# Kernel optimization log

Hardware: AMD Instinct MI355X
Metric: run time of the kernel (lower is better)

Reference implementation:

```python
import jax, jax.numpy as jnp
import numpy as np

KEY_DIM, VALUE_DIM, N_ACTIONS = 128, 64, 256
B, L = 32, 2048


def setup_inputs() -> dict:
    key = jax.random.key(0)
    k1, k2, k3 = jax.random.split(key, 3)
    key_vectors = jax.random.normal(k1, (B, L, KEY_DIM), dtype=jnp.float32)
    value_vectors = jax.random.normal(k2, (B, N_ACTIONS, KEY_DIM), dtype=jnp.float32)
    weights = jax.random.normal(k3, (KEY_DIM, VALUE_DIM, N_ACTIONS), dtype=jnp.float32)
    return {"key_vectors": key_vectors, "value_vectors": value_vectors, "weights": weights}


def reference(key_vectors, value_vectors, weights):
    # torch: einsum('bln,nka->bla', key, W) sums over both n (key_dim) and k (value_dim)
    scores = jnp.einsum('bln,nka->bla', key_vectors, weights)  # (B, L, A)
    # fused multiply-then-reduce over actions == batched matmul (no (B,L,A,D) intermediate)
    mem_vectors = jnp.einsum('bla,bad->bld', scores, value_vectors)  # (B, L, key_dim)
    q_values = jnp.einsum('bln,bmn->blm', key_vectors, mem_vectors)  # (B, L, L)
    return q_values
```

## Files before the change

### kernel.cpp

```cpp
#include <hip/hip_runtime.h>
#include <hip/hip_bf16.h>

#define KD 128
#define VD 64
#define NA 256
#define NB 32
#define LL 2048

typedef __attribute__((ext_vector_type(8))) short bf16x8;
typedef __attribute__((ext_vector_type(4))) float f32x4;
typedef __attribute__((ext_vector_type(8))) unsigned short u16x8;
typedef __attribute__((ext_vector_type(4))) unsigned short u16x4;

static __device__ __forceinline__ unsigned short f2bf(float x) {
  __hip_bfloat16 h = __float2bfloat16(x);
  unsigned short u;
  __builtin_memcpy(&u, &h, 2);
  return u;
}

static __device__ __forceinline__ void stage16(const void* gsrc, void* ldst) {
  __builtin_amdgcn_global_load_lds(
      (const __attribute__((address_space(1))) void*)gsrc,
      (__attribute__((address_space(3))) void*)ldst, 16, 0, 0);
}

__global__ __launch_bounds__(256) void fold_w(const float* __restrict__ W,
                                              float* __restrict__ W2) {
  const int idx = blockIdx.x * 256 + threadIdx.x;
  const int n = idx >> 8, a = idx & 255;
  const float* p = W + (long)n * (VD * NA) + a;
  float s = 0.f;
  #pragma unroll
  for (int k = 0; k < VD; ++k) s += p[k * NA];
  W2[idx] = s;
}

__global__ __launch_bounds__(128) void compute_t(const float* __restrict__ W2,
                                                 const float* __restrict__ V,
                                                 unsigned short* __restrict__ Tt) {
  const int n = threadIdx.x;
  const int d0 = blockIdx.x * 8;
  const int b = blockIdx.y;
  const float* vb = V + (long)b * NA * KD + d0;
  const float* w2p = W2 + n * NA;
  float acc[8] = {0.f, 0.f, 0.f, 0.f, 0.f, 0.f, 0.f, 0.f};
  for (int a = 0; a < NA; a += 4) {
    const float4 w = *(const float4*)(w2p + a);
    const float wq[4] = {w.x, w.y, w.z, w.w};
    #pragma unroll
    for (int q = 0; q < 4; ++q) {
      const float* vr = vb + (long)(a + q) * KD;
      #pragma unroll
      for (int j = 0; j < 8; ++j) acc[j] += wq[q] * vr[j];
    }
  }
  #pragma unroll
  for (int j = 0; j < 8; ++j)
    Tt[((long)b * KD + d0 + j) * KD + n] = f2bf(acc[j]);
}

__global__ __launch_bounds__(256) void cvt_key(const float* __restrict__ in,
                                               unsigned short* __restrict__ out) {
  const long i = ((long)blockIdx.x * 256 + threadIdx.x) * 8;
  const float4 f0 = *(const float4*)(in + i);
  const float4 f1 = *(const float4*)(in + i + 4);
  u16x8 r;
  r[0] = f2bf(f0.x); r[1] = f2bf(f0.y); r[2] = f2bf(f0.z); r[3] = f2bf(f0.w);
  r[4] = f2bf(f1.x); r[5] = f2bf(f1.y); r[6] = f2bf(f1.z); r[7] = f2bf(f1.w);
  *(u16x8*)(out + i) = r;
}

__global__ __launch_bounds__(256) void gemm_mem(const unsigned short* __restrict__ A,
                                                const unsigned short* __restrict__ Bm,
                                                unsigned short* __restrict__ C) {
  __shared__ unsigned short lds[32768];
  const int nper = gridDim.x >> 3;
  const int lg = (blockIdx.x & 7) * nper + (blockIdx.x >> 3);
  const int mt = lg & 15;
  const int b = lg >> 4;

  const int tid = threadIdx.x;
  const int lane = tid & 63, w = tid >> 6;
  const int l15 = lane & 15, lhi = lane >> 4;

  const unsigned short* gA = A + ((long)b * LL + mt * 128) * KD;
  const unsigned short* gB = Bm + (long)b * KD * KD;

  unsigned short* ldsA = lds;
  unsigned short* ldsB = lds + 16384;

  #pragma unroll
  for (int i = 0; i < 8; ++i) {
    const int addr = (w * 8 + i) * 1024 + lane * 16;
    const int row = addr >> 8;
    const int src = addr ^ ((row & 7) << 4);
    stage16((const char*)gA + src, (char*)ldsA + addr);
    stage16((const char*)gB + src, (char*)ldsB + addr);
  }
  __syncthreads();

  const int wr = w >> 1, wc = w & 1;
  f32x4 acc[4][4];
  #pragma unroll
  for (int i = 0; i < 4; ++i)
    #pragma unroll
    for (int j = 0; j < 4; ++j) acc[i][j] = f32x4{0.f, 0.f, 0.f, 0.f};

  #pragma unroll
  for (int ks = 0; ks < 4; ++ks) {
    const int kb = (ks * 32 + lhi * 8) * 2;
    bf16x8 av[4], bv[4];
    #pragma unroll
    for (int mf = 0; mf < 4; ++mf) {
      const int row = wr * 64 + mf * 16 + l15;
      const int byte = (row * 256 + kb) ^ ((row & 7) << 4);
      av[mf] = *(const bf16x8*)((const char*)ldsA + byte);
    }
    #pragma unroll
    for (int nf = 0; nf < 4; ++nf) {
      const int row = wc * 64 + nf * 16 + l15;
      const int byte = (row * 256 + kb) ^ ((row & 7) << 4);
      bv[nf] = *(const bf16x8*)((const char*)ldsB + byte);
    }
    #pragma unroll
    for (int mf = 0; mf < 4; ++mf)
      #pragma unroll
      for (int nf = 0; nf < 4; ++nf)
        acc[mf][nf] = __builtin_amdgcn_mfma_f32_16x16x32_bf16(bv[nf], av[mf],
                                                              acc[mf][nf], 0, 0, 0);
  }

  const long row0 = (long)b * LL + mt * 128 + wr * 64;
  const int col0 = wc * 64;
  #pragma unroll
  for (int mf = 0; mf < 4; ++mf)
    #pragma unroll
    for (int nf = 0; nf < 4; ++nf) {
      const long r = row0 + mf * 16 + l15;
      const int c = col0 + nf * 16 + lhi * 4;
      u16x4 v;
      #pragma unroll
      for (int i = 0; i < 4; ++i) v[i] = f2bf(acc[mf][nf][i]);
      *(u16x4*)(C + r * KD + c) = v;
    }
}

__global__ __launch_bounds__(512, 2) void gemm_q(const unsigned short* __restrict__ A,
                                                 const unsigned short* __restrict__ Bm,
                                                 float* __restrict__ C) {
  __shared__ unsigned short lds[65536];

  const int lg = (blockIdx.x & 7) * 256 + (blockIdx.x >> 3);
  const int nt = lg & 7;
  const int mt = (lg >> 3) & 7;
  const int b = lg >> 6;

  const int tid = threadIdx.x;
  const int lane = tid & 63, w = tid >> 6;
  const int l15 = lane & 15, lhi = lane >> 4;
  const int wrM = w >> 2;
  const int wcN = w & 3;

  const unsigned short* gA = A + ((long)b * LL + mt * 256) * KD;
  const unsigned short* gB = Bm + ((long)b * LL + nt * 256) * KD;

  unsigned short* ldsA = lds;
  unsigned short* ldsB = lds + 32768;

  #pragma unroll
  for (int i = 0; i < 8; ++i) {
    const int addr = i * 8192 + tid * 16;
    const int row = addr >> 8;
    const int src = addr ^ ((row & 7) << 4);
    stage16((const char*)gA + src, (char*)ldsA + addr);
    stage16((const char*)gB + src, (char*)ldsB + addr);
  }
  __syncthreads();

  f32x4 acc[8][4];
  #pragma unroll
  for (int i = 0; i < 8; ++i)
    #pragma unroll
    for (int j = 0; j < 4; ++j) acc[i][j] = f32x4{0.f, 0.f, 0.f, 0.f};

  #pragma unroll
  for (int ks = 0; ks < 4; ++ks) {
    const int kb = (ks * 32 + lhi * 8) * 2;
    bf16x8 av[8], bv[4];
    #pragma unroll
    for (int mf = 0; mf < 8; ++mf) {
      const int row = wrM * 128 + mf * 16 + l15;
      const int byte = (row * 256 + kb) ^ ((row & 7) << 4);
      av[mf] = *(const bf16x8*)((const char*)ldsA + byte);
    }
    #pragma unroll
    for (int nf = 0; nf < 4; ++nf) {
      const int row = wcN * 64 + nf * 16 + l15;
      const int byte = (row * 256 + kb) ^ ((row & 7) << 4);
      bv[nf] = *(const bf16x8*)((const char*)ldsB + byte);
    }
    #pragma unroll
    for (int mf = 0; mf < 8; ++mf)
      #pragma unroll
      for (int nf = 0; nf < 4; ++nf)
        acc[mf][nf] = __builtin_amdgcn_mfma_f32_16x16x32_bf16(bv[nf], av[mf],
                                                              acc[mf][nf], 0, 0, 0);
  }

  const long row0 = (long)b * LL + mt * 256 + wrM * 128;
  const int col0 = nt * 256 + wcN * 64;
  #pragma unroll
  for (int mf = 0; mf < 8; ++mf)
    #pragma unroll
    for (int nf = 0; nf < 4; ++nf) {
      const long r = row0 + mf * 16 + l15;
      const int c = col0 + nf * 16 + lhi * 4;
      *(f32x4*)(C + r * LL + c) = acc[mf][nf];
    }
}

extern "C" void kernel_launch(void* const* d_in, const int* in_sizes, int n_in,
                              void* d_out, int out_size, void* d_ws, size_t ws_size,
                              hipStream_t stream) {
  const float* key = (const float*)d_in[0];
  const float* val = (const float*)d_in[1];
  const float* wts = (const float*)d_in[2];
  float* out = (float*)d_out;

  char* ws = (char*)d_ws;
  float* W2 = (float*)ws;
  unsigned short* Tt = (unsigned short*)(ws + 131072);
  unsigned short* keyB = (unsigned short*)(ws + 131072 + 1048576);
  unsigned short* memB = (unsigned short*)(ws + 131072 + 1048576 + 16777216);

  fold_w<<<128, 256, 0, stream>>>(wts, W2);
  compute_t<<<dim3(16, NB), 128, 0, stream>>>(W2, val, Tt);
  cvt_key<<<4096, 256, 0, stream>>>(key, keyB);
  gemm_mem<<<16 * NB, 256, 0, stream>>>(keyB, Tt, memB);
  gemm_q<<<8 * 8 * NB, 512, 0, stream>>>(keyB, memB, out);
}
```

Baseline: 177.3 us.

## Make gemm_q persistent over M tiles, overlapping next A-tile load with stores

Each gemm_q block now keeps its B tile resident and loops over all eight M tiles of the batch, instead of launching one block per (M,N) tile. The next A tile is prefetched into LDS with global_load_lds while the current fp32 output tile is being written, so load latency is meant to hide behind the store-bound epilogue. This cuts the grid from 2048 to 256 blocks, which may underfill the CUs. The vmcnt-based wait also relies on an exact count of in-flight stores and loads.

```diff
diff --git a/kernel.cpp b/kernel.cpp
--- a/kernel.cpp
+++ b/kernel.cpp
@@ -149,12 +149,12 @@
 __global__ __launch_bounds__(512, 2) void gemm_q(const unsigned short* __restrict__ A,
                                                  const unsigned short* __restrict__ Bm,
                                                  float* __restrict__ C) {
-  __shared__ unsigned short lds[65536];
-
-  const int lg = (blockIdx.x & 7) * 256 + (blockIdx.x >> 3);
+  __shared__ unsigned short ldsA[32768];
+  __shared__ unsigned short ldsB[32768];
+
+  const int lg = (blockIdx.x & 7) * 32 + (blockIdx.x >> 3);
   const int nt = lg & 7;
-  const int mt = (lg >> 3) & 7;
-  const int b = lg >> 6;
+  const int b = lg >> 3;
 
   const int tid = threadIdx.x;
   const int lane = tid & 63, w = tid >> 6;
@@ -162,62 +162,87 @@
   const int wrM = w >> 2;
   const int wcN = w & 3;
 
-  const unsigned short* gA = A + ((long)b * LL + mt * 256) * KD;
   const unsigned short* gB = Bm + ((long)b * LL + nt * 256) * KD;
-
-  unsigned short* ldsA = lds;
-  unsigned short* ldsB = lds + 32768;
+  const unsigned short* gAb = A + (long)b * LL * KD;
 
   #pragma unroll
   for (int i = 0; i < 8; ++i) {
     const int addr = i * 8192 + tid * 16;
     const int row = addr >> 8;
     const int src = addr ^ ((row & 7) << 4);
-    stage16((const char*)gA + src, (char*)ldsA + addr);
     stage16((const char*)gB + src, (char*)ldsB + addr);
-  }
-  __syncthreads();
-
-  f32x4 acc[8][4];
-  #pragma unroll
-  for (int i = 0; i < 8; ++i)
-    #pragma unroll
-    for (int j = 0; j < 4; ++j) acc[i][j] = f32x4{0.f, 0.f, 0.f, 0.f};
-
-  #pragma unroll
-  for (int ks = 0; ks < 4; ++ks) {
-    const int kb = (ks * 32 + lhi * 8) * 2;
-    bf16x8 av[8], bv[4];
-    #pragma unroll
-    for (int mf = 0; mf < 8; ++mf) {
-      const int row = wrM * 128 + mf * 16 + l15;
-      const int byte = (row * 256 + kb) ^ ((row & 7) << 4);
-      av[mf] = *(const bf16x8*)((const char*)ldsA + byte);
-    }
-    #pragma unroll
-    for (int nf = 0; nf < 4; ++nf) {
-      const int row = wcN * 64 + nf * 16 + l15;
-      const int byte = (row * 256 + kb) ^ ((row & 7) << 4);
-      bv[nf] = *(const bf16x8*)((const char*)ldsB + byte);
-    }
+    stage16((const char*)gAb + src, (char*)ldsA + addr);
+  }
+  asm volatile("s_waitcnt vmcnt(0)" ::: "memory");
+  __builtin_amdgcn_s_barrier();
+  __builtin_amdgcn_sched_barrier(0);
+
+  const int col0 = nt * 256 + wcN * 64;
+
+  for (int mt = 0; mt < 8; ++mt) {
+    f32x4 acc[8][4];
+    #pragma unroll
+    for (int i = 0; i < 8; ++i)
+      #pragma unroll
+      for (int j = 0; j < 4; ++j) acc[i][j] = f32x4{0.f, 0.f, 0.f, 0.f};
+
+    #pragma unroll
+    for (int ks = 0; ks < 4; ++ks) {
+      const int kb = (ks * 32 + lhi * 8) * 2;
+      bf16x8 av[8], bv[4];
+      #pragma unroll
+      for (int mf = 0; mf < 8; ++mf) {
+        const int row = wrM * 128 + mf * 16 + l15;
+        const int byte = (row * 256 + kb) ^ ((row & 7) << 4);
+        av[mf] = *(const bf16x8*)((const char*)ldsA + byte);
+      }
+      #pragma unroll
+      for (int nf = 0; nf < 4; ++nf) {
+        const int row = wcN * 64 + nf * 16 + l15;
+        const int byte = (row * 256 + kb) ^ ((row & 7) << 4);
+        bv[nf] = *(const bf16x8*)((const char*)ldsB + byte);
+      }
+      #pragma unroll
+      for (int mf = 0; mf < 8; ++mf)
+        #pragma unroll
+        for (int nf = 0; nf < 4; ++nf)
+          acc[mf][nf] = __builtin_amdgcn_mfma_f32_16x16x32_bf16(bv[nf], av[mf],
+                                                                acc[mf][nf], 0, 0, 0);
+    }
+
+    asm volatile("s_waitcnt lgkmcnt(0)" ::: "memory");
+    __builtin_amdgcn_s_barrier();
+    __builtin_amdgcn_sched_barrier(0);
+
+    if (mt < 7) {
+      const char* gA = (const char*)(gAb + (long)(mt + 1) * 256 * KD);
+      #pragma unroll
+      for (int i = 0; i < 8; ++i) {
+        const int addr = i * 8192 + tid * 16;
+        const int row = addr >> 8;
+        const int src = addr ^ ((row & 7) << 4);
+        stage16(gA + src, (char*)ldsA + addr);
+      }
+    }
+    __builtin_amdgcn_sched_barrier(0);
+
+    const long row0 = (long)b * LL + mt * 256 + wrM * 128;
     #pragma unroll
     for (int mf = 0; mf < 8; ++mf)
       #pragma unroll
-      for (int nf = 0; nf < 4; ++nf)
-        acc[mf][nf] = __builtin_amdgcn_mfma_f32_16x16x32_bf16(bv[nf], av[mf],
-                                                              acc[mf][nf], 0, 0, 0);
-  }
-
-  const long row0 = (long)b * LL + mt * 256 + wrM * 128;
-  const int col0 = nt * 256 + wcN * 64;
-  #pragma unroll
-  for (int mf = 0; mf < 8; ++mf)
-    #pragma unroll
-    for (int nf = 0; nf < 4; ++nf) {
-      const long r = row0 + mf * 16 + l15;
-      const int c = col0 + nf * 16 + lhi * 4;
-      *(f32x4*)(C + r * LL + c) = acc[mf][nf];
-    }
+      for (int nf = 0; nf < 4; ++nf) {
+        const long r = row0 + mf * 16 + l15;
+        const int c = col0 + nf * 16 + lhi * 4;
+        *(f32x4*)(C + r * LL + c) = acc[mf][nf];
+      }
+
+    if (mt < 7) {
+      asm volatile("s_waitcnt vmcnt(32)" ::: "memory");
+      __builtin_amdgcn_sched_barrier(0);
+      __builtin_amdgcn_s_barrier();
+      __builtin_amdgcn_sched_barrier(0);
+    }
+  }
 }
 
 extern "C" void kernel_launch(void* const* d_in, const int* in_sizes, int n_in,
@@ -238,5 +263,5 @@
   compute_t<<<dim3(16, NB), 128, 0, stream>>>(W2, val, Tt);
   cvt_key<<<4096, 256, 0, stream>>>(key, keyB);
   gemm_mem<<<16 * NB, 256, 0, stream>>>(keyB, Tt, memB);
-  gemm_q<<<8 * 8 * NB, 512, 0, stream>>>(keyB, memB, out);
-}
+  gemm_q<<<8 * NB, 512, 0, stream>>>(keyB, memB, out);
+}
```

New measurement: 165.5 us. -6.7%, faster.
